# Kernel optimization log

Measured on AMD Instinct MI355X. Metric: run time of the kernel, lower is better.

The kernel has to match this reference:

```python
import jax, jax.numpy as jnp
import numpy as np

N_TOKENS = 16384
D_MODEL = 2048
NUM_EXPERTS = 64
TOPK = 8


def setup_inputs() -> dict:
    key = jax.random.key(0)
    k_x, k_eps, k_wg, k_wn = jax.random.split(key, 4)
    scale = 1.0 / np.sqrt(D_MODEL)  # nn.Linear-style init scale
    return {
        "x": jax.random.normal(k_x, (N_TOKENS, D_MODEL), dtype=jnp.float32),
        "noise_eps": jax.random.normal(k_eps, (N_TOKENS, NUM_EXPERTS), dtype=jnp.float32),
        "Wg": jax.random.normal(k_wg, (D_MODEL, NUM_EXPERTS), dtype=jnp.float32) * scale,
        "bg": jnp.zeros((NUM_EXPERTS,), dtype=jnp.float32),
        "Wn": jax.random.normal(k_wn, (D_MODEL, NUM_EXPERTS), dtype=jnp.float32) * scale,
        "bn": jnp.zeros((NUM_EXPERTS,), dtype=jnp.float32),
    }


def reference(x, noise_eps, Wg, bg, Wn, bn):
    # logits = gate_linear(x); noise_std = softplus(noise_linear(x))
    logits = x @ Wg + bg                      # [N, E]
    noise_std = jax.nn.softplus(x @ Wn + bn)  # [N, E]
    noisy_logit = logits + noise_eps * noise_std

    # top-k over experts, then scatter into a -inf-filled tensor
    topk_logits, indices = jax.lax.top_k(noisy_logit, TOPK)  # [N, k], [N, k]
    neg_inf = jnp.array(-jnp.inf, dtype=noisy_logit.dtype)
    sparse_logits = jnp.full_like(noisy_logit, neg_inf)
    rows = jnp.arange(noisy_logit.shape[0])[:, None]          # [N, 1]
    sparse_logits = sparse_logits.at[rows, indices].set(topk_logits)

    # softmax over experts; non-topk entries (-inf) become exactly 0
    router_output = jax.nn.softmax(sparse_logits, axis=-1)
    return router_output, indices
```

## Files before the change

### kernel.cpp

```cpp
#include <hip/hip_runtime.h>
#include <math.h>

#define N_TOKENS 16384
#define D_MODEL  2048
#define NE       64
#define TOPK     8

typedef float f32x4 __attribute__((ext_vector_type(4)));
typedef short s16x8 __attribute__((ext_vector_type(8)));

#define LDSROW 40
#define PLANE  (16 * LDSROW)
#define XS_BUF (3 * PLANE)
#define ACC_LD 129

__device__ __forceinline__ float bf16_rne(float v, short* s) {
    unsigned u = __float_as_uint(v);
    unsigned r = (u + 0x7fffu + ((u >> 16) & 1u)) & 0xffff0000u;
    *s = (short)(r >> 16);
    return __uint_as_float(r);
}

__global__ __launch_bounds__(256)
void bf_build(const float* __restrict__ Wg, const float* __restrict__ Wn,
              s16x8* __restrict__ BF) {
    const int id  = blockIdx.x * 256 + threadIdx.x;
    const int l   = id & 63;
    const int s   = (id >> 6) % 3;
    const int ctc = (id >> 6) / 3;
    const int ct  = ctc & 7;
    const int c   = ctc >> 3;
    const int k0  = c * 32 + (l >> 4) * 8;
    const int col = ct * 16 + (l & 15);
    const float* W = (col < NE) ? (Wg + col) : (Wn + (col - NE));
    s16x8 o;
    #pragma unroll
    for (int e = 0; e < 8; ++e) {
        float v  = W[(size_t)(k0 + e) * NE];
        short h, m, lo;
        float hf = bf16_rne(v, &h);
        float r1 = v - hf;
        float mf = bf16_rne(r1, &m);
        float r2 = r1 - mf;
        bf16_rne(r2, &lo);
        o[e] = (s == 0) ? h : (s == 1) ? m : lo;
    }
    BF[id] = o;
}

__global__ __launch_bounds__(512, 8)
void router_mfma(const float* __restrict__ x, const float* __restrict__ eps,
                 const s16x8* __restrict__ BF, const float* __restrict__ bg,
                 const float* __restrict__ bn, float* __restrict__ out_probs,
                 float* __restrict__ out_idx)
{
    __shared__ char smem[16 * ACC_LD * 8];
    short*  xsp = (short*)smem;
    double* acc = (double*)smem;

    const int tid  = threadIdx.x;
    const int lane = tid & 63;
    const int wv   = tid >> 6;
    const int row0 = blockIdx.x * 16;

    const int crow = tid >> 5;
    const int ck   = tid & 31;
    const float* xp = x + (size_t)(row0 + crow) * D_MODEL + ck;
    const int cbase = crow * LDSROW + ck;

    auto convert_store = [&](float v, int bb) {
        short h, m, l;
        float hf = bf16_rne(v, &h);
        float r1 = v - hf;
        float mf = bf16_rne(r1, &m);
        bf16_rne(r1 - mf, &l);
        short* xb = xsp + bb * XS_BUF;
        xb[cbase]             = h;
        xb[cbase + PLANE]     = m;
        xb[cbase + 2 * PLANE] = l;
    };

    const int abase = (lane & 15) * LDSROW + (lane >> 4) * 8;
    const s16x8* bfp = BF + lane;

    f32x4  C = {0.f, 0.f, 0.f, 0.f};
    double facc[4] = {0.0, 0.0, 0.0, 0.0};

    auto do_chunk = [&](int c, int bb) {
        s16x8 Bv[3];
        #pragma unroll
        for (int s = 0; s < 3; ++s)
            Bv[s] = bfp[(size_t)(((c * 8) + wv) * 3 + s) * 64];
        const short* xb = xsp + bb * XS_BUF;
        s16x8 Ah = *(const s16x8*)&xb[abase];
        s16x8 Am = *(const s16x8*)&xb[abase + PLANE];
        s16x8 Al = *(const s16x8*)&xb[abase + 2 * PLANE];
        C = __builtin_amdgcn_mfma_f32_16x16x32_bf16(Am, Bv[1], C, 0, 0, 0);
        C = __builtin_amdgcn_mfma_f32_16x16x32_bf16(Ah, Bv[2], C, 0, 0, 0);
        C = __builtin_amdgcn_mfma_f32_16x16x32_bf16(Al, Bv[0], C, 0, 0, 0);
        C = __builtin_amdgcn_mfma_f32_16x16x32_bf16(Ah, Bv[1], C, 0, 0, 0);
        C = __builtin_amdgcn_mfma_f32_16x16x32_bf16(Am, Bv[0], C, 0, 0, 0);
        C = __builtin_amdgcn_mfma_f32_16x16x32_bf16(Ah, Bv[0], C, 0, 0, 0);
    };

    #define CONVOY_BARRIER() do {                                   \
        asm volatile("s_waitcnt lgkmcnt(0)" ::: "memory");          \
        __builtin_amdgcn_s_barrier();                               \
        __builtin_amdgcn_sched_barrier(0);                          \
    } while (0)

    convert_store(xp[0], 0);
    float xa, xb4;
    xb4 = xp[32];
    CONVOY_BARRIER();

    #pragma unroll 1
    for (int c = 0; c < 64; c += 2) {
        if (c + 2 < 64) xa = xp[(c + 2) * 32];
        convert_store(xb4, 1);
        do_chunk(c, 0);
        CONVOY_BARRIER();

        if (c + 3 < 64) xb4 = xp[(c + 3) * 32];
        if (c + 2 < 64) convert_store(xa, 0);
        do_chunk(c + 1, 1);
        #pragma unroll
        for (int j = 0; j < 4; ++j) { facc[j] += (double)C[j]; C[j] = 0.f; }
        CONVOY_BARRIER();
    }

    __syncthreads();

    #pragma unroll
    for (int j = 0; j < 4; ++j)
        acc[(size_t)((lane >> 4) * 4 + j) * ACC_LD + wv * 16 + (lane & 15)] = facc[j];
    __syncthreads();

    const float bgv = bg[lane];
    const float bnv = bn[lane];

    #pragma unroll 1
    for (int q = 0; q < 2; ++q) {
        const int tt  = wv * 2 + q;
        const int tok = row0 + tt;
        const double logit = acc[(size_t)tt * ACC_LD + lane] + (double)bgv;
        const double nvv   = acc[(size_t)tt * ACC_LD + 64 + lane] + (double)bnv;
        const double sp    = (nvv > 0.0) ? (nvv + log1p(exp(-nvv))) : log1p(exp(nvv));
        const double noisy = logit + (double)eps[(size_t)tok * NE + lane] * sp;

        double cur = noisy;
        double m = 0.0, sum = 0.0;
        int    sel = 0;
        float  my_idx = 0.0f;
        #pragma unroll
        for (int rk = 0; rk < TOPK; ++rk) {
            double bv = cur;
            int    bi = lane;
            #pragma unroll
            for (int off = 32; off >= 1; off >>= 1) {
                double ov = __shfl_xor(bv, off);
                int    oi = __shfl_xor(bi, off);
                if (ov > bv || (ov == bv && oi < bi)) { bv = ov; bi = oi; }
            }
            if (rk == 0) m = bv;
            sum += exp(bv - m);
            if (lane == bi) { sel = 1; cur = -INFINITY; }
            if (lane == rk) my_idx = (float)bi;
        }

        out_probs[(size_t)tok * NE + lane] = (float)(sel ? exp(noisy - m) / sum : 0.0);
        if (lane < TOPK) out_idx[(size_t)tok * TOPK + lane] = my_idx;
    }
}

extern "C" void kernel_launch(void* const* d_in, const int* in_sizes, int n_in,
                              void* d_out, int out_size, void* d_ws, size_t ws_size,
                              hipStream_t stream) {
    const float* x   = (const float*)d_in[0];
    const float* eps = (const float*)d_in[1];
    const float* Wg  = (const float*)d_in[2];
    const float* bg  = (const float*)d_in[3];
    const float* Wn  = (const float*)d_in[4];
    const float* bn  = (const float*)d_in[5];

    float* out_probs = (float*)d_out;
    float* out_idx   = (float*)d_out + (size_t)N_TOKENS * NE;

    s16x8* BF = (s16x8*)d_ws;

    bf_build<<<dim3(384), dim3(256), 0, stream>>>(Wg, Wn, BF);

    router_mfma<<<dim3(N_TOKENS / 16), dim3(512), 0, stream>>>(
        x, eps, BF, bg, bn, out_probs, out_idx);
}
```

Measured before the change: 129.0 us.

## Prefetch B fragments a chunk ahead and split MFMA accumulator chains

Preloads the bf16-split weight fragments one chunk ahead into register double buffers, and splits the six dependent MFMAs across three independent accumulators to shorten the dependency chain. It also changes the LDS row stride to 34 and loosens launch bounds from 8 to 4 waves-per-EU hint, and prefetches x two chunks ahead with clamped indices. The aim is to hide global load latency and MFMA back-to-back dependency stalls, at the cost of more registers and possibly lower occupancy. The LDS padding change may alter bank conflicts for the 16-byte A reads, and the final iteration still does an unused convert_store into buffer 0.

```diff
diff --git a/kernel.cpp b/kernel.cpp
--- a/kernel.cpp
+++ b/kernel.cpp
@@ -9,7 +9,7 @@
 typedef float f32x4 __attribute__((ext_vector_type(4)));
 typedef short s16x8 __attribute__((ext_vector_type(8)));
 
-#define LDSROW 40
+#define LDSROW 34
 #define PLANE  (16 * LDSROW)
 #define XS_BUF (3 * PLANE)
 #define ACC_LD 129
@@ -48,7 +48,7 @@
     BF[id] = o;
 }
 
-__global__ __launch_bounds__(512, 8)
+__global__ __launch_bounds__(512, 4)
 void router_mfma(const float* __restrict__ x, const float* __restrict__ eps,
                  const s16x8* __restrict__ BF, const float* __restrict__ bg,
                  const float* __restrict__ bn, float* __restrict__ out_probs,
@@ -83,24 +83,26 @@
     const int abase = (lane & 15) * LDSROW + (lane >> 4) * 8;
     const s16x8* bfp = BF + lane;
 
-    f32x4  C = {0.f, 0.f, 0.f, 0.f};
-    double facc[4] = {0.0, 0.0, 0.0, 0.0};
-
-    auto do_chunk = [&](int c, int bb) {
-        s16x8 Bv[3];
+    auto loadB = [&](int c, s16x8* dst) {
         #pragma unroll
         for (int s = 0; s < 3; ++s)
-            Bv[s] = bfp[(size_t)(((c * 8) + wv) * 3 + s) * 64];
+            dst[s] = bfp[(size_t)(((c * 8) + wv) * 3 + s) * 64];
+    };
+
+    f32x4 Ca = {0.f,0.f,0.f,0.f}, Cb = Ca, Cc = Ca;
+    double facc[4] = {0.0, 0.0, 0.0, 0.0};
+
+    auto do_chunk = [&](const s16x8* Bv, int bb) {
         const short* xb = xsp + bb * XS_BUF;
         s16x8 Ah = *(const s16x8*)&xb[abase];
         s16x8 Am = *(const s16x8*)&xb[abase + PLANE];
         s16x8 Al = *(const s16x8*)&xb[abase + 2 * PLANE];
-        C = __builtin_amdgcn_mfma_f32_16x16x32_bf16(Am, Bv[1], C, 0, 0, 0);
-        C = __builtin_amdgcn_mfma_f32_16x16x32_bf16(Ah, Bv[2], C, 0, 0, 0);
-        C = __builtin_amdgcn_mfma_f32_16x16x32_bf16(Al, Bv[0], C, 0, 0, 0);
-        C = __builtin_amdgcn_mfma_f32_16x16x32_bf16(Ah, Bv[1], C, 0, 0, 0);
-        C = __builtin_amdgcn_mfma_f32_16x16x32_bf16(Am, Bv[0], C, 0, 0, 0);
-        C = __builtin_amdgcn_mfma_f32_16x16x32_bf16(Ah, Bv[0], C, 0, 0, 0);
+        Ca = __builtin_amdgcn_mfma_f32_16x16x32_bf16(Am, Bv[1], Ca, 0, 0, 0);
+        Cb = __builtin_amdgcn_mfma_f32_16x16x32_bf16(Ah, Bv[2], Cb, 0, 0, 0);
+        Cc = __builtin_amdgcn_mfma_f32_16x16x32_bf16(Al, Bv[0], Cc, 0, 0, 0);
+        Ca = __builtin_amdgcn_mfma_f32_16x16x32_bf16(Ah, Bv[1], Ca, 0, 0, 0);
+        Cb = __builtin_amdgcn_mfma_f32_16x16x32_bf16(Am, Bv[0], Cb, 0, 0, 0);
+        Cc = __builtin_amdgcn_mfma_f32_16x16x32_bf16(Ah, Bv[0], Cc, 0, 0, 0);
     };
 
     #define CONVOY_BARRIER() do {                                   \
@@ -109,23 +111,31 @@
         __builtin_amdgcn_sched_barrier(0);                          \
     } while (0)
 
+    s16x8 Bcur[3], Bnext[3];
     convert_store(xp[0], 0);
-    float xa, xb4;
-    xb4 = xp[32];
+    float u = xp[32];
+    float v = xp[64];
+    loadB(0, Bcur);
+    loadB(1, Bnext);
     CONVOY_BARRIER();
 
     #pragma unroll 1
     for (int c = 0; c < 64; c += 2) {
-        if (c + 2 < 64) xa = xp[(c + 2) * 32];
-        convert_store(xb4, 1);
-        do_chunk(c, 0);
+        convert_store(u, 1);
+        u = xp[min(c + 3, 63) * 32];
+        do_chunk(Bcur, 0);
+        loadB(min(c + 2, 63), Bcur);
         CONVOY_BARRIER();
 
-        if (c + 3 < 64) xb4 = xp[(c + 3) * 32];
-        if (c + 2 < 64) convert_store(xa, 0);
-        do_chunk(c + 1, 1);
+        convert_store(v, 0);
+        v = xp[min(c + 4, 63) * 32];
+        do_chunk(Bnext, 1);
+        loadB(min(c + 3, 63), Bnext);
         #pragma unroll
-        for (int j = 0; j < 4; ++j) { facc[j] += (double)C[j]; C[j] = 0.f; }
+        for (int j = 0; j < 4; ++j) {
+            facc[j] += (double)Ca[j] + (double)Cb[j] + (double)Cc[j];
+            Ca[j] = 0.f; Cb[j] = 0.f; Cc[j] = 0.f;
+        }
         CONVOY_BARRIER();
     }
 
```

Result: slower. 232.2 us (+80.0%).

## Switch split-precision GEMM from 3-way bf16 to scaled 2-way fp16 with deeper pipeline

Applied to the files above, without the earlier changes.

Splits x and the weights into two scaled fp16 parts instead of three bf16 parts, dropping from six MFMAs per chunk to three and shrinking the LDS footprint and weight-buffer traffic. Scale factors keep values inside fp16 range, and the result is unscaled after accumulation. The main loop now processes four chunks per iteration with a four-slot LDS ring, prefetching B fragments into registers two chunks ahead, and occupancy hints drop from 8 to 6. Precision is somewhat lower than the three-term bf16 split, which could change top-k selection on near-ties.

```diff
diff --git a/kernel.cpp b/kernel.cpp
--- a/kernel.cpp
+++ b/kernel.cpp
@@ -1,4 +1,5 @@
 #include <hip/hip_runtime.h>
+#include <hip/hip_fp16.h>
 #include <math.h>
 
 #define N_TOKENS 16384
@@ -6,28 +7,25 @@
 #define NE       64
 #define TOPK     8
 
-typedef float f32x4 __attribute__((ext_vector_type(4)));
-typedef short s16x8 __attribute__((ext_vector_type(8)));
-
-#define LDSROW 40
+typedef float    f32x4 __attribute__((ext_vector_type(4)));
+typedef _Float16 f16x8 __attribute__((ext_vector_type(8)));
+typedef short    s16x8 __attribute__((ext_vector_type(8)));
+
+#define LDSROW 34
 #define PLANE  (16 * LDSROW)
-#define XS_BUF (3 * PLANE)
+#define CH_BUF (2 * PLANE)
 #define ACC_LD 129
-
-__device__ __forceinline__ float bf16_rne(float v, short* s) {
-    unsigned u = __float_as_uint(v);
-    unsigned r = (u + 0x7fffu + ((u >> 16) & 1u)) & 0xffff0000u;
-    *s = (short)(r >> 16);
-    return __uint_as_float(r);
-}
+#define WSCL   512.0f
+#define XSCL   1024.0f
+#define UNSCL  (1.0 / (1024.0 * 512.0))
 
 __global__ __launch_bounds__(256)
 void bf_build(const float* __restrict__ Wg, const float* __restrict__ Wn,
               s16x8* __restrict__ BF) {
     const int id  = blockIdx.x * 256 + threadIdx.x;
     const int l   = id & 63;
-    const int s   = (id >> 6) % 3;
-    const int ctc = (id >> 6) / 3;
+    const int s   = (id >> 6) & 1;
+    const int ctc = id >> 7;
     const int ct  = ctc & 7;
     const int c   = ctc >> 3;
     const int k0  = c * 32 + (l >> 4) * 8;
@@ -36,19 +34,15 @@
     s16x8 o;
     #pragma unroll
     for (int e = 0; e < 8; ++e) {
-        float v  = W[(size_t)(k0 + e) * NE];
-        short h, m, lo;
-        float hf = bf16_rne(v, &h);
-        float r1 = v - hf;
-        float mf = bf16_rne(r1, &m);
-        float r2 = r1 - mf;
-        bf16_rne(r2, &lo);
-        o[e] = (s == 0) ? h : (s == 1) ? m : lo;
+        float v  = W[(size_t)(k0 + e) * NE] * WSCL;
+        __half h = __float2half(v);
+        if (s == 0) o[e] = __half_as_short(h);
+        else        o[e] = __half_as_short(__float2half(v - __half2float(h)));
     }
     BF[id] = o;
 }
 
-__global__ __launch_bounds__(512, 8)
+__global__ __launch_bounds__(512, 6)
 void router_mfma(const float* __restrict__ x, const float* __restrict__ eps,
                  const s16x8* __restrict__ BF, const float* __restrict__ bg,
                  const float* __restrict__ bn, float* __restrict__ out_probs,
@@ -68,39 +62,35 @@
     const float* xp = x + (size_t)(row0 + crow) * D_MODEL + ck;
     const int cbase = crow * LDSROW + ck;
 
-    auto convert_store = [&](float v, int bb) {
-        short h, m, l;
-        float hf = bf16_rne(v, &h);
-        float r1 = v - hf;
-        float mf = bf16_rne(r1, &m);
-        bf16_rne(r1 - mf, &l);
-        short* xb = xsp + bb * XS_BUF;
-        xb[cbase]             = h;
-        xb[cbase + PLANE]     = m;
-        xb[cbase + 2 * PLANE] = l;
+    auto convert_store = [&](float vf, int c) {
+        float v  = vf * XSCL;
+        __half h = __float2half(v);
+        float  r = v - __half2float(h);
+        __half m = __float2half(r);
+        short* xb = xsp + (c & 3) * CH_BUF;
+        xb[cbase]         = __half_as_short(h);
+        xb[cbase + PLANE] = __half_as_short(m);
     };
 
     const int abase = (lane & 15) * LDSROW + (lane >> 4) * 8;
-    const s16x8* bfp = BF + lane;
-
-    f32x4  C = {0.f, 0.f, 0.f, 0.f};
+    const f16x8* bfp = (const f16x8*)BF + lane;
+
+    auto loadB = [&](int c, f16x8& bh, f16x8& bm) {
+        const f16x8* p = bfp + (size_t)((c * 8 + wv) * 2) * 64;
+        bh = p[0];
+        bm = p[64];
+    };
+
+    f32x4 Ca = {0.f,0.f,0.f,0.f}, Cb = Ca;
     double facc[4] = {0.0, 0.0, 0.0, 0.0};
 
-    auto do_chunk = [&](int c, int bb) {
-        s16x8 Bv[3];
-        #pragma unroll
-        for (int s = 0; s < 3; ++s)
-            Bv[s] = bfp[(size_t)(((c * 8) + wv) * 3 + s) * 64];
-        const short* xb = xsp + bb * XS_BUF;
-        s16x8 Ah = *(const s16x8*)&xb[abase];
-        s16x8 Am = *(const s16x8*)&xb[abase + PLANE];
-        s16x8 Al = *(const s16x8*)&xb[abase + 2 * PLANE];
-        C = __builtin_amdgcn_mfma_f32_16x16x32_bf16(Am, Bv[1], C, 0, 0, 0);
-        C = __builtin_amdgcn_mfma_f32_16x16x32_bf16(Ah, Bv[2], C, 0, 0, 0);
-        C = __builtin_amdgcn_mfma_f32_16x16x32_bf16(Al, Bv[0], C, 0, 0, 0);
-        C = __builtin_amdgcn_mfma_f32_16x16x32_bf16(Ah, Bv[1], C, 0, 0, 0);
-        C = __builtin_amdgcn_mfma_f32_16x16x32_bf16(Am, Bv[0], C, 0, 0, 0);
-        C = __builtin_amdgcn_mfma_f32_16x16x32_bf16(Ah, Bv[0], C, 0, 0, 0);
+    auto do_chunk = [&](f16x8 Bh, f16x8 Bm, int c) {
+        const short* xb = xsp + (c & 3) * CH_BUF;
+        f16x8 Ah = *(const f16x8*)&xb[abase];
+        f16x8 Am = *(const f16x8*)&xb[abase + PLANE];
+        Ca = __builtin_amdgcn_mfma_f32_16x16x32_f16(Am, Bh, Ca, 0, 0, 0);
+        Cb = __builtin_amdgcn_mfma_f32_16x16x32_f16(Ah, Bm, Cb, 0, 0, 0);
+        Ca = __builtin_amdgcn_mfma_f32_16x16x32_f16(Ah, Bh, Ca, 0, 0, 0);
     };
 
     #define CONVOY_BARRIER() do {                                   \
@@ -109,23 +99,38 @@
         __builtin_amdgcn_sched_barrier(0);                          \
     } while (0)
 
+    f16x8 B0h,B0m,B1h,B1m,B2h,B2m,B3h,B3m;
+    float u0, u1, u2, u3;
     convert_store(xp[0], 0);
-    float xa, xb4;
-    xb4 = xp[32];
+    convert_store(xp[32], 1);
+    u0 = xp[2 * 32]; u1 = xp[3 * 32];
+    loadB(0, B0h, B0m); loadB(1, B1h, B1m);
     CONVOY_BARRIER();
 
     #pragma unroll 1
-    for (int c = 0; c < 64; c += 2) {
-        if (c + 2 < 64) xa = xp[(c + 2) * 32];
-        convert_store(xb4, 1);
-        do_chunk(c, 0);
+    for (int m = 0; m < 64; m += 4) {
+        loadB(min(m + 2, 63), B2h, B2m);
+        loadB(min(m + 3, 63), B3h, B3m);
+        u2 = xp[min(m + 4, 63) * 32];
+        u3 = xp[min(m + 5, 63) * 32];
+        convert_store(u0, m + 2);
+        convert_store(u1, m + 3);
+        do_chunk(B0h, B0m, m);
+        do_chunk(B1h, B1m, m + 1);
+        #pragma unroll
+        for (int j = 0; j < 4; ++j) { facc[j] += (double)Ca[j] + (double)Cb[j]; Ca[j] = 0.f; Cb[j] = 0.f; }
         CONVOY_BARRIER();
 
-        if (c + 3 < 64) xb4 = xp[(c + 3) * 32];
-        if (c + 2 < 64) convert_store(xa, 0);
-        do_chunk(c + 1, 1);
+        loadB(min(m + 4, 63), B0h, B0m);
+        loadB(min(m + 5, 63), B1h, B1m);
+        u0 = xp[min(m + 6, 63) * 32];
+        u1 = xp[min(m + 7, 63) * 32];
+        convert_store(u2, min(m + 4, 63));
+        convert_store(u3, min(m + 5, 63));
+        do_chunk(B2h, B2m, m + 2);
+        do_chunk(B3h, B3m, m + 3);
         #pragma unroll
-        for (int j = 0; j < 4; ++j) { facc[j] += (double)C[j]; C[j] = 0.f; }
+        for (int j = 0; j < 4; ++j) { facc[j] += (double)Ca[j] + (double)Cb[j]; Ca[j] = 0.f; Cb[j] = 0.f; }
         CONVOY_BARRIER();
     }
 
@@ -133,7 +138,7 @@
 
     #pragma unroll
     for (int j = 0; j < 4; ++j)
-        acc[(size_t)((lane >> 4) * 4 + j) * ACC_LD + wv * 16 + (lane & 15)] = facc[j];
+        acc[(size_t)((lane >> 4) * 4 + j) * ACC_LD + wv * 16 + (lane & 15)] = facc[j] * UNSCL;
     __syncthreads();
 
     const float bgv = bg[lane];
@@ -188,7 +193,7 @@
 
     s16x8* BF = (s16x8*)d_ws;
 
-    bf_build<<<dim3(384), dim3(256), 0, stream>>>(Wg, Wn, BF);
+    bf_build<<<dim3(256), dim3(256), 0, stream>>>(Wg, Wn, BF);
 
     router_mfma<<<dim3(N_TOKENS / 16), dim3(512), 0, stream>>>(
         x, eps, BF, bg, bn, out_probs, out_idx);
```

New measurement: 168.6 us. 30.7% more time.
